# Optimization experiments

Measured on AMD Instinct MI355X. Metric: run time of the kernel, lower is better.

## Reference

```python
import jax, jax.numpy as jnp
import numpy as np

N_NODES = 100000
N_EDGES = 600000
FEAT = 128
HID = 128
N_LAYERS = 5
BN_EPS = 1e-5


def setup_inputs() -> dict:
    key = jax.random.key(0)
    ks = jax.random.split(key, 10)
    x = jax.random.normal(ks[0], (N_NODES, FEAT), dtype=jnp.float32)
    edge_index = jax.random.randint(ks[1], (2, N_EDGES), 0, N_NODES, dtype=jnp.int64)
    # conv weights: all layers are 128->128 (glorot-ish scale)
    conv_w = jax.random.normal(ks[2], (N_LAYERS, HID, HID), dtype=jnp.float32) * (1.0 / np.sqrt(HID))
    conv_b = jnp.zeros((N_LAYERS, HID), dtype=jnp.float32)
    bn_gamma = jnp.ones((N_LAYERS, HID), dtype=jnp.float32)
    bn_beta = jnp.zeros((N_LAYERS, HID), dtype=jnp.float32)
    fc_w = jax.random.normal(ks[3], (1, HID), dtype=jnp.float32) * (1.0 / np.sqrt(HID))
    fc_b = jnp.zeros((1,), dtype=jnp.float32)
    return {"x": x, "edge_index": edge_index, "conv_w": conv_w, "conv_b": conv_b,
            "bn_gamma": bn_gamma, "bn_beta": bn_beta, "fc_w": fc_w, "fc_b": fc_b}


def _gcn_norm(edge_index, n_nodes):
    # PyG gcn_norm with add_self_loops=True, edge_weight=None (ones)
    row = jnp.concatenate([edge_index[0], jnp.arange(n_nodes, dtype=edge_index.dtype)])
    col = jnp.concatenate([edge_index[1], jnp.arange(n_nodes, dtype=edge_index.dtype)])
    ew = jnp.ones(row.shape[0], dtype=jnp.float32)
    deg = jax.ops.segment_sum(ew, col, num_segments=n_nodes)
    dinv = jnp.where(deg > 0, jax.lax.rsqrt(deg), 0.0)
    norm = dinv[row] * ew * dinv[col]  # [E + N]
    return row, col, norm


def reference(x, edge_index, conv_w, conv_b, bn_gamma, bn_beta, fc_w, fc_b):
    n = x.shape[0]
    row, col, norm = _gcn_norm(edge_index, n)
    for l in range(N_LAYERS):
        h = x @ conv_w[l]                                   # [N, H]
        msg = norm[:, None] * h[row]                        # gather + scale
        h = jax.ops.segment_sum(msg, col, num_segments=n)   # scatter-add
        h = h + conv_b[l]
        # BatchNorm1d (training-mode batch stats, biased var)
        mean = jnp.mean(h, axis=0)
        var = jnp.var(h, axis=0)
        h = bn_gamma[l] * (h - mean) * jax.lax.rsqrt(var + BN_EPS) + bn_beta[l]
        x = jax.nn.relu(h)
    edge_emb = x[edge_index[0]] * x[edge_index[1]]          # [E, H]
    out = edge_emb @ fc_w.T + fc_b                          # [E, 1]
    return jax.nn.sigmoid(out)
```

## Files before the change

kernel.cpp:

```cpp
#include <hip/hip_runtime.h>

#define NN 100000
#define NE 600000
#define HH 128
#define NL 5
#define BN_EPS 1e-5f
#define NB 391
#define NBS 782
#define L2B 32
#define RPB 25

typedef float f4 __attribute__((ext_vector_type(4)));
typedef float f2 __attribute__((ext_vector_type(2)));
typedef _Float16 h8 __attribute__((ext_vector_type(8)));
typedef _Float16 h2x __attribute__((ext_vector_type(2)));

__global__ void k_probe(const unsigned long long* __restrict__ e, int* __restrict__ flag) {
    if (blockIdx.x == 0 && threadIdx.x == 0) {
        int ok = 1;
        for (int i = 0; i < 64; ++i)
            if (e[i] >= (unsigned long long)NN) ok = 0;
        *flag = ok;
    }
}

__global__ void k_convert(const void* __restrict__ src, const int* __restrict__ flag,
                          int* __restrict__ dst) {
    int i = blockIdx.x * 256 + threadIdx.x;
    if (i >= 2 * NE) return;
    if (*flag) dst[i] = (int)((const long long*)src)[i];
    else       dst[i] = ((const int*)src)[i];
}

__global__ void k_zero(int* __restrict__ p, int n) {
    int i = blockIdx.x * 256 + threadIdx.x;
    if (i < n) p[i] = 0;
}

__global__ void k_count_deg(const int* __restrict__ col, int* __restrict__ degi) {
    int e = blockIdx.x * 256 + threadIdx.x;
    if (e < NE) atomicAdd(&degi[col[e]], 1);
}

__global__ void k_dinv(const int* __restrict__ degi, float* __restrict__ dinv) {
    int i = blockIdx.x * 256 + threadIdx.x;
    if (i < NN) dinv[i] = rsqrtf((float)degi[i] + 1.0f);
}

__global__ __launch_bounds__(256) void k_scan1(const int* __restrict__ degi,
                                               int* __restrict__ incl,
                                               int* __restrict__ blocksums) {
    __shared__ int sd[256];
    int tid = threadIdx.x;
    int i = blockIdx.x * 256 + tid;
    int v = (i < NN) ? degi[i] : 0;
    sd[tid] = v;
    __syncthreads();
#pragma unroll
    for (int off = 1; off < 256; off <<= 1) {
        int t = (tid >= off) ? sd[tid - off] : 0;
        __syncthreads();
        sd[tid] += t;
        __syncthreads();
    }
    if (i < NN) incl[i] = sd[tid];
    if (tid == 255) blocksums[blockIdx.x] = sd[255];
}

__global__ __launch_bounds__(512) void k_scan2(const int* __restrict__ blocksums,
                                               int* __restrict__ blockoffs) {
    __shared__ int sd[512];
    int tid = threadIdx.x;
    int v = (tid < NB) ? blocksums[tid] : 0;
    sd[tid] = v;
    __syncthreads();
#pragma unroll
    for (int off = 1; off < 512; off <<= 1) {
        int t = (tid >= off) ? sd[tid - off] : 0;
        __syncthreads();
        sd[tid] += t;
        __syncthreads();
    }
    if (tid < NB) blockoffs[tid] = sd[tid] - v;
}

__global__ void k_scan3(const int* __restrict__ incl, const int* __restrict__ degi,
                        const int* __restrict__ blockoffs,
                        int* __restrict__ offsets, int* __restrict__ cursor) {
    int i = blockIdx.x * 256 + threadIdx.x;
    if (i >= NN) return;
    offsets[i] = incl[i] - degi[i] + blockoffs[blockIdx.x];
    cursor[i] = 0;
}

__global__ void k_scatter(const int* __restrict__ ei, const float* __restrict__ dinv,
                          const int* __restrict__ offsets, int* __restrict__ cursor,
                          int2* __restrict__ csr) {
    int e = blockIdx.x * 256 + threadIdx.x;
    if (e >= NE) return;
    int r = ei[e], c = ei[NE + e];
    int pos = offsets[c] + atomicAdd(&cursor[c], 1);
    int2 v;
    v.x = r;
    v.y = __float_as_int(dinv[r] * dinv[c]);
    csr[pos] = v;
}

__global__ void k_wt(const float* __restrict__ W, _Float16* __restrict__ Wt_hi,
                     _Float16* __restrict__ Wt_lo) {
    int gid = blockIdx.x * 256 + threadIdx.x;
    if (gid >= NL * HH * HH) return;
    int l = gid >> 14;
    int rem = gid & 16383;
    int n = rem >> 7;
    int k = rem & 127;
    float w = W[l * HH * HH + k * HH + n];
    _Float16 hi = (_Float16)w;
    _Float16 lo = (_Float16)(w - (float)hi);
    Wt_hi[gid] = hi;
    Wt_lo[gid] = lo;
}

__global__ void k_prep(const float* __restrict__ stats, const float* __restrict__ gamma,
                       const float* __restrict__ beta, int mode, float* __restrict__ scsh) {
    int k = threadIdx.x;
    float sc = 1.0f, sh = 0.0f;
    if (mode) {
        const float inv_n = 1.0f / (float)NN;
        float mean = stats[k] * inv_n;
        float var  = stats[128 + k] * inv_n - mean * mean;
        sc = gamma[k] * rsqrtf(var + BN_EPS);
        sh = beta[k] - mean * sc;
    }
    scsh[k] = sc;
    scsh[128 + k] = sh;
}

__global__ __launch_bounds__(256) void k_gemm(const float* __restrict__ A,
                                              const _Float16* __restrict__ Wt_hi,
                                              const _Float16* __restrict__ Wt_lo,
                                              const float* __restrict__ scsh,
                                              float negmul,
                                              float* __restrict__ C) {
    __shared__ _Float16 sBH[16384];
    __shared__ _Float16 sBL[16384];
    const int tid = threadIdx.x;

#pragma unroll
    for (int it = 0; it < 8; ++it) {
        int g  = it * 256 + tid;
        int rr = g & 15;
        int kg = (g >> 4) & 3;
        int kc = (g >> 6) & 3;
        int n  = g >> 8;
        int glob = (n * 16 + rr) * HH + kc * 32 + kg * 8;
        *reinterpret_cast<h8*>(&sBH[g * 8]) = *reinterpret_cast<const h8*>(Wt_hi + glob);
        *reinterpret_cast<h8*>(&sBL[g * 8]) = *reinterpret_cast<const h8*>(Wt_lo + glob);
    }
    __syncthreads();

    const int wave = tid >> 6;
    const int lane = tid & 63;
    const int r    = lane & 15;
    const int kg   = lane >> 4;
    const int row0 = blockIdx.x * 256 + wave * 64;

    f4 acc[4][8];
#pragma unroll
    for (int m = 0; m < 4; ++m)
#pragma unroll
        for (int n = 0; n < 8; ++n) acc[m][n] = (f4)0.0f;

    const float* Ap[4];
#pragma unroll
    for (int m = 0; m < 4; ++m) {
        int ra = row0 + m * 16 + r;
        if (ra >= NN) ra = NN - 1;
        Ap[m] = A + (size_t)ra * HH + kg * 8;
    }

#pragma unroll
    for (int kc = 0; kc < 4; ++kc) {
        const int k0 = kc * 32 + kg * 8;
        f4 scA = *reinterpret_cast<const f4*>(scsh + k0);
        f4 scB = *reinterpret_cast<const f4*>(scsh + k0 + 4);
        f4 shA = *reinterpret_cast<const f4*>(scsh + 128 + k0);
        f4 shB = *reinterpret_cast<const f4*>(scsh + 128 + k0 + 4);
        h8 ahi[4], alo[4];
#pragma unroll
        for (int m = 0; m < 4; ++m) {
            f4 ax = *reinterpret_cast<const f4*>(Ap[m] + kc * 32);
            f4 ay = *reinterpret_cast<const f4*>(Ap[m] + kc * 32 + 4);
#pragma unroll
            for (int j = 0; j < 4; ++j) {
                float t;
                t = fmaf(ax[j], scA[j], shA[j]); t = fmaxf(t, t * negmul);
                ahi[m][j] = (_Float16)t;      alo[m][j] = (_Float16)(t - (float)ahi[m][j]);
                t = fmaf(ay[j], scB[j], shB[j]); t = fmaxf(t, t * negmul);
                ahi[m][j + 4] = (_Float16)t;  alo[m][j + 4] = (_Float16)(t - (float)ahi[m][j + 4]);
            }
        }
#pragma unroll
        for (int n = 0; n < 8; ++n) {
            int g = n * 256 + kc * 64 + lane;
            h8 bh = *reinterpret_cast<const h8*>(&sBH[g * 8]);
            h8 bl = *reinterpret_cast<const h8*>(&sBL[g * 8]);
#pragma unroll
            for (int m = 0; m < 4; ++m) {
                acc[m][n] = __builtin_amdgcn_mfma_f32_16x16x32_f16(bh, ahi[m], acc[m][n], 0, 0, 0);
                acc[m][n] = __builtin_amdgcn_mfma_f32_16x16x32_f16(bl, ahi[m], acc[m][n], 0, 0, 0);
                acc[m][n] = __builtin_amdgcn_mfma_f32_16x16x32_f16(bh, alo[m], acc[m][n], 0, 0, 0);
            }
        }
    }

#pragma unroll
    for (int m = 0; m < 4; ++m) {
        int rr = row0 + m * 16 + r;
        if (rr < NN) {
            float* Crow = C + (size_t)rr * HH + kg * 4;
#pragma unroll
            for (int n = 0; n < 8; ++n)
                *reinterpret_cast<f4*>(Crow + n * 16) = acc[m][n];
        }
    }
}

__global__ __launch_bounds__(256) void k_gather(const float* __restrict__ h1,
                                                const int* __restrict__ offsets,
                                                const int* __restrict__ degi,
                                                const int2* __restrict__ csr,
                                                const float* __restrict__ dinv,
                                                float* __restrict__ h2) {
    int gid  = blockIdx.x * 256 + threadIdx.x;
    int node = gid >> 6;
    int lane = gid & 63;
    if (node >= NN) return;
    float di = dinv[node];
    f2 acc0 = reinterpret_cast<const f2*>(h1 + (size_t)node * HH)[lane] * (di * di);
    f2 acc1 = (f2)0.0f, acc2 = (f2)0.0f, acc3 = (f2)0.0f;
    const int start = offsets[node];
    const int end   = start + degi[node];
    for (int b = start; b < end; b += 4) {
        int2 ce0 = csr[b];
        int2 ce1 = (b + 1 < end) ? csr[b + 1] : make_int2(0, 0);
        int2 ce2 = (b + 2 < end) ? csr[b + 2] : make_int2(0, 0);
        int2 ce3 = (b + 3 < end) ? csr[b + 3] : make_int2(0, 0);
        f2 v0 = reinterpret_cast<const f2*>(h1 + (size_t)ce0.x * HH)[lane];
        f2 v1 = reinterpret_cast<const f2*>(h1 + (size_t)ce1.x * HH)[lane];
        f2 v2 = reinterpret_cast<const f2*>(h1 + (size_t)ce2.x * HH)[lane];
        f2 v3 = reinterpret_cast<const f2*>(h1 + (size_t)ce3.x * HH)[lane];
        acc0 += v0 * __int_as_float(ce0.y);
        acc1 += v1 * __int_as_float(ce1.y);
        acc2 += v2 * __int_as_float(ce2.y);
        acc3 += v3 * __int_as_float(ce3.y);
    }
    acc0 += acc2;
    acc1 += acc3;
    acc0 += acc1;
    reinterpret_cast<f2*>(h2 + (size_t)node * HH)[lane] = acc0;
}

__global__ __launch_bounds__(256) void k_bnstats(const float* __restrict__ h,
                                                 float* __restrict__ partial) {
    __shared__ f4 ls[8][32];
    __shared__ f4 lss[8][32];
    const int q  = threadIdx.x & 31;
    const int rg = threadIdx.x >> 5;
    const int r0 = blockIdx.x * 128;
    int rend = r0 + 128;
    if (rend > NN) rend = NN;
    f4 s = (f4)0.0f, ss = (f4)0.0f;
    for (int r = r0 + rg; r < rend; r += 8) {
        f4 v = *reinterpret_cast<const f4*>(h + (size_t)r * HH + q * 4);
        s += v;
        ss += v * v;
    }
    ls[rg][q] = s;
    lss[rg][q] = ss;
    __syncthreads();
    if (rg == 0) {
        f4 st = ls[0][q];
#pragma unroll
        for (int g = 1; g < 8; ++g) st += ls[g][q];
        *reinterpret_cast<f4*>(&partial[(size_t)blockIdx.x * 256 + q * 4]) = st;
    } else if (rg == 1) {
        f4 sq = lss[0][q];
#pragma unroll
        for (int g = 1; g < 8; ++g) sq += lss[g][q];
        *reinterpret_cast<f4*>(&partial[(size_t)blockIdx.x * 256 + 128 + q * 4]) = sq;
    }
}

__global__ void k_sred1(const float* __restrict__ partial, float* __restrict__ level2) {
    int c = threadIdx.x;
    int b0 = blockIdx.x * RPB;
    int b1 = b0 + RPB;
    if (b1 > NBS) b1 = NBS;
    float s = 0.0f;
    for (int b = b0; b < b1; ++b) s += partial[(size_t)b * 256 + c];
    level2[(size_t)blockIdx.x * 256 + c] = s;
}

__global__ void k_sred2(const float* __restrict__ level2, float* __restrict__ stats) {
    int c = threadIdx.x;
    float s = 0.0f;
#pragma unroll
    for (int b = 0; b < L2B; ++b) s += level2[(size_t)b * 256 + c];
    stats[c] = s;
}

__global__ void k_bnapply(const float* __restrict__ h2, const float* __restrict__ stats,
                          const float* __restrict__ gamma, const float* __restrict__ beta,
                          _Float16* __restrict__ xh) {
    int idx = blockIdx.x * 256 + threadIdx.x;
    if (idx >= NN * 64) return;
    int cp = idx & 63;
    int c0 = 2 * cp, c1 = c0 + 1;
    const float inv_n = 1.0f / (float)NN;
    float m0 = stats[c0] * inv_n, m1 = stats[c1] * inv_n;
    float v0s = stats[128 + c0] * inv_n - m0 * m0;
    float v1s = stats[128 + c1] * inv_n - m1 * m1;
    float sc0 = gamma[c0] * rsqrtf(v0s + BN_EPS);
    float sc1 = gamma[c1] * rsqrtf(v1s + BN_EPS);
    float sh0 = beta[c0] - m0 * sc0;
    float sh1 = beta[c1] - m1 * sc1;
    f2 v = reinterpret_cast<const f2*>(h2)[idx];
    float t0 = fmaf(v[0], sc0, sh0);
    float t1 = fmaf(v[1], sc1, sh1);
    t0 = fmaxf(t0, 0.0f);
    t1 = fmaxf(t1, 0.0f);
    h2x o;
    o[0] = (_Float16)t0;
    o[1] = (_Float16)t1;
    reinterpret_cast<h2x*>(xh)[idx] = o;
}

__global__ __launch_bounds__(256) void k_final(const _Float16* __restrict__ x,
                                               const int* __restrict__ ei,
                                               const float* __restrict__ fcw,
                                               const float* __restrict__ fcb,
                                               float* __restrict__ out) {
    int gid  = blockIdx.x * 256 + threadIdx.x;
    int e    = gid >> 4;
    int l16  = gid & 15;
    if (e >= NE) return;
    int a = ei[e];
    int b = ei[NE + e];
    h8 va = *reinterpret_cast<const h8*>(x + (size_t)a * HH + l16 * 8);
    h8 vb = *reinterpret_cast<const h8*>(x + (size_t)b * HH + l16 * 8);
    f4 w0 = *reinterpret_cast<const f4*>(fcw + l16 * 8);
    f4 w1 = *reinterpret_cast<const f4*>(fcw + l16 * 8 + 4);
    float p = 0.0f;
#pragma unroll
    for (int j = 0; j < 4; ++j) {
        p += (float)va[j] * (float)vb[j] * w0[j];
        p += (float)va[j + 4] * (float)vb[j + 4] * w1[j];
    }
#pragma unroll
    for (int off = 8; off > 0; off >>= 1) p += __shfl_xor(p, off, 64);
    if (l16 == 0) out[e] = 1.0f / (1.0f + expf(-(p + fcb[0])));
}

extern "C" void kernel_launch(void* const* d_in, const int* in_sizes, int n_in,
                              void* d_out, int out_size, void* d_ws, size_t ws_size,
                              hipStream_t stream) {
    const float* x   = (const float*)d_in[0];
    const void*  ei_raw = d_in[1];
    const float* cw  = (const float*)d_in[2];
    const float* gam = (const float*)d_in[4];
    const float* bet = (const float*)d_in[5];
    const float* fcw = (const float*)d_in[6];
    const float* fcb = (const float*)d_in[7];
    float* out = (float*)d_out;

    const size_t NH = (size_t)NN * HH;
    unsigned char* p = (unsigned char*)d_ws;
    float* h1 = (float*)p;       p += NH * 4;
    float* h2 = (float*)p;       p += NH * 4;
    _Float16* xh = (_Float16*)p; p += NH * 2;
    _Float16* WtH = (_Float16*)p; p += (size_t)NL * HH * HH * 2;
    _Float16* WtL = (_Float16*)p; p += (size_t)NL * HH * HH * 2;
    int2*  csr   = (int2*)p;     p += (size_t)NE * 8;
    float* dinv  = (float*)p;    p += NN * 4;
    float* stats = (float*)p;    p += NL * 256 * 4;
    float* scsh  = (float*)p;    p += NL * 256 * 4;
    float* partial = (float*)p;  p += (size_t)NBS * 256 * 4;
    float* level2  = (float*)p;  p += (size_t)L2B * 256 * 4;
    int*   ei    = (int*)p;      p += (size_t)2 * NE * 4;
    int*   degi  = (int*)p;      p += NN * 4;
    int*   incl  = (int*)p;      p += NN * 4;
    int*   offsets = (int*)p;    p += NN * 4;
    int*   cursor  = (int*)p;    p += NN * 4;
    int*   blocksums = (int*)p;  p += NB * 4;
    int*   blockoffs = (int*)p;  p += NB * 4;
    int*   flag  = (int*)p;

    k_probe<<<1, 64, 0, stream>>>((const unsigned long long*)ei_raw, flag);
    k_convert<<<(2 * NE + 255) / 256, 256, 0, stream>>>(ei_raw, flag, ei);

    k_zero<<<(NN + 255) / 256, 256, 0, stream>>>(degi, NN);
    k_count_deg<<<(NE + 255) / 256, 256, 0, stream>>>(ei + NE, degi);
    k_dinv<<<(NN + 255) / 256, 256, 0, stream>>>(degi, dinv);
    k_scan1<<<NB, 256, 0, stream>>>(degi, incl, blocksums);
    k_scan2<<<1, 512, 0, stream>>>(blocksums, blockoffs);
    k_scan3<<<NB, 256, 0, stream>>>(incl, degi, blockoffs, offsets, cursor);
    k_scatter<<<(NE + 255) / 256, 256, 0, stream>>>(ei, dinv, offsets, cursor, csr);

    k_wt<<<(NL * HH * HH + 255) / 256, 256, 0, stream>>>(cw, WtH, WtL);

    for (int l = 0; l < NL; ++l) {
        k_prep<<<1, 128, 0, stream>>>(
            (l == 0) ? stats : stats + (size_t)(l - 1) * 256,
            (l == 0) ? gam : gam + (size_t)(l - 1) * HH,
            (l == 0) ? bet : bet + (size_t)(l - 1) * HH,
            (l == 0) ? 0 : 1, scsh + (size_t)l * 256);
        k_gemm<<<(NN + 255) / 256, 256, 0, stream>>>(
            (l == 0) ? x : h2, WtH + (size_t)l * HH * HH, WtL + (size_t)l * HH * HH,
            scsh + (size_t)l * 256, (l == 0) ? 1.0f : 0.0f, h1);
        k_gather<<<(NN * 64 + 255) / 256, 256, 0, stream>>>(h1, offsets, degi, csr, dinv, h2);
        k_bnstats<<<NBS, 256, 0, stream>>>(h2, partial);
        k_sred1<<<L2B, 256, 0, stream>>>(partial, level2);
        k_sred2<<<1, 256, 0, stream>>>(level2, stats + (size_t)l * 256);
    }
    k_bnapply<<<(NN * 64 + 255) / 256, 256, 0, stream>>>(h2, stats + (size_t)(NL - 1) * 256,
                                                         gam + (size_t)(NL - 1) * HH,
                                                         bet + (size_t)(NL - 1) * HH, xh);
    k_final<<<(NE * 16 + 255) / 256, 256, 0, stream>>>(xh, ei, fcw, fcb, out);
}
```

Measured before the change: 690.8 us.

## Fuse BatchNorm statistics into gather kernel and fold final reduction into prep

The gather kernel now computes per-block sums and squared sums of its output rows in shared memory and writes a partial per block, which removes the separate bnstats pass that re-read h2 each layer. The second-level reduction is folded into k_prep, and bnapply now reads precomputed scale and shift values, which drops the sred2 launches. The cost is that sred1 must now reduce 25000 partials instead of 782, using only 32 blocks of long serial loops. The gather kernel also gains a __syncthreads barrier.

```diff
diff --git a/kernel.cpp b/kernel.cpp
--- a/kernel.cpp
+++ b/kernel.cpp
@@ -6,9 +6,9 @@
 #define NL 5
 #define BN_EPS 1e-5f
 #define NB 391
-#define NBS 782
+#define NGB 25000
 #define L2B 32
-#define RPB 25
+#define RPB2 782
 
 typedef float f4 __attribute__((ext_vector_type(4)));
 typedef float f2 __attribute__((ext_vector_type(2)));
@@ -121,14 +121,20 @@
     Wt_lo[gid] = lo;
 }
 
-__global__ void k_prep(const float* __restrict__ stats, const float* __restrict__ gamma,
+__global__ void k_prep(const float* __restrict__ level2, const float* __restrict__ gamma,
                        const float* __restrict__ beta, int mode, float* __restrict__ scsh) {
     int k = threadIdx.x;
     float sc = 1.0f, sh = 0.0f;
     if (mode) {
+        float s = 0.0f, q = 0.0f;
+#pragma unroll
+        for (int b = 0; b < L2B; ++b) {
+            s += level2[(size_t)b * 256 + k];
+            q += level2[(size_t)b * 256 + 128 + k];
+        }
         const float inv_n = 1.0f / (float)NN;
-        float mean = stats[k] * inv_n;
-        float var  = stats[128 + k] * inv_n - mean * mean;
+        float mean = s * inv_n;
+        float var  = q * inv_n - mean * mean;
         sc = gamma[k] * rsqrtf(var + BN_EPS);
         sh = beta[k] - mean * sc;
     }
@@ -231,11 +237,14 @@
                                                 const int* __restrict__ degi,
                                                 const int2* __restrict__ csr,
                                                 const float* __restrict__ dinv,
-                                                float* __restrict__ h2) {
+                                                float* __restrict__ h2,
+                                                float* __restrict__ partial) {
+    __shared__ f2 ls[4][64];
+    __shared__ f2 lss[4][64];
     int gid  = blockIdx.x * 256 + threadIdx.x;
     int node = gid >> 6;
     int lane = gid & 63;
-    if (node >= NN) return;
+    int wid  = threadIdx.x >> 6;
     float di = dinv[node];
     f2 acc0 = reinterpret_cast<const f2*>(h1 + (size_t)node * HH)[lane] * (di * di);
     f2 acc1 = (f2)0.0f, acc2 = (f2)0.0f, acc3 = (f2)0.0f;
@@ -259,72 +268,37 @@
     acc1 += acc3;
     acc0 += acc1;
     reinterpret_cast<f2*>(h2 + (size_t)node * HH)[lane] = acc0;
-}
-
-__global__ __launch_bounds__(256) void k_bnstats(const float* __restrict__ h,
-                                                 float* __restrict__ partial) {
-    __shared__ f4 ls[8][32];
-    __shared__ f4 lss[8][32];
-    const int q  = threadIdx.x & 31;
-    const int rg = threadIdx.x >> 5;
-    const int r0 = blockIdx.x * 128;
-    int rend = r0 + 128;
-    if (rend > NN) rend = NN;
-    f4 s = (f4)0.0f, ss = (f4)0.0f;
-    for (int r = r0 + rg; r < rend; r += 8) {
-        f4 v = *reinterpret_cast<const f4*>(h + (size_t)r * HH + q * 4);
-        s += v;
-        ss += v * v;
-    }
-    ls[rg][q] = s;
-    lss[rg][q] = ss;
+
+    ls[wid][lane] = acc0;
+    lss[wid][lane] = acc0 * acc0;
     __syncthreads();
-    if (rg == 0) {
-        f4 st = ls[0][q];
-#pragma unroll
-        for (int g = 1; g < 8; ++g) st += ls[g][q];
-        *reinterpret_cast<f4*>(&partial[(size_t)blockIdx.x * 256 + q * 4]) = st;
-    } else if (rg == 1) {
-        f4 sq = lss[0][q];
-#pragma unroll
-        for (int g = 1; g < 8; ++g) sq += lss[g][q];
-        *reinterpret_cast<f4*>(&partial[(size_t)blockIdx.x * 256 + 128 + q * 4]) = sq;
+    if (threadIdx.x < 64) {
+        int c = threadIdx.x;
+        f2 s = ls[0][c] + ls[1][c] + ls[2][c] + ls[3][c];
+        f2 q = lss[0][c] + lss[1][c] + lss[2][c] + lss[3][c];
+        f2* pp = reinterpret_cast<f2*>(partial + (size_t)blockIdx.x * 256);
+        pp[c] = s;
+        pp[64 + c] = q;
     }
 }
 
 __global__ void k_sred1(const float* __restrict__ partial, float* __restrict__ level2) {
     int c = threadIdx.x;
-    int b0 = blockIdx.x * RPB;
-    int b1 = b0 + RPB;
-    if (b1 > NBS) b1 = NBS;
+    int b0 = blockIdx.x * RPB2;
+    int b1 = b0 + RPB2;
+    if (b1 > NGB) b1 = NGB;
     float s = 0.0f;
     for (int b = b0; b < b1; ++b) s += partial[(size_t)b * 256 + c];
     level2[(size_t)blockIdx.x * 256 + c] = s;
 }
 
-__global__ void k_sred2(const float* __restrict__ level2, float* __restrict__ stats) {
-    int c = threadIdx.x;
-    float s = 0.0f;
-#pragma unroll
-    for (int b = 0; b < L2B; ++b) s += level2[(size_t)b * 256 + c];
-    stats[c] = s;
-}
-
-__global__ void k_bnapply(const float* __restrict__ h2, const float* __restrict__ stats,
-                          const float* __restrict__ gamma, const float* __restrict__ beta,
+__global__ void k_bnapply(const float* __restrict__ h2, const float* __restrict__ scsh,
                           _Float16* __restrict__ xh) {
     int idx = blockIdx.x * 256 + threadIdx.x;
     if (idx >= NN * 64) return;
     int cp = idx & 63;
-    int c0 = 2 * cp, c1 = c0 + 1;
-    const float inv_n = 1.0f / (float)NN;
-    float m0 = stats[c0] * inv_n, m1 = stats[c1] * inv_n;
-    float v0s = stats[128 + c0] * inv_n - m0 * m0;
-    float v1s = stats[128 + c1] * inv_n - m1 * m1;
-    float sc0 = gamma[c0] * rsqrtf(v0s + BN_EPS);
-    float sc1 = gamma[c1] * rsqrtf(v1s + BN_EPS);
-    float sh0 = beta[c0] - m0 * sc0;
-    float sh1 = beta[c1] - m1 * sc1;
+    float sc0 = scsh[2 * cp],       sc1 = scsh[2 * cp + 1];
+    float sh0 = scsh[128 + 2 * cp], sh1 = scsh[128 + 2 * cp + 1];
     f2 v = reinterpret_cast<const f2*>(h2)[idx];
     float t0 = fmaf(v[0], sc0, sh0);
     float t1 = fmaf(v[1], sc1, sh1);
@@ -383,9 +357,8 @@
     _Float16* WtL = (_Float16*)p; p += (size_t)NL * HH * HH * 2;
     int2*  csr   = (int2*)p;     p += (size_t)NE * 8;
     float* dinv  = (float*)p;    p += NN * 4;
-    float* stats = (float*)p;    p += NL * 256 * 4;
-    float* scsh  = (float*)p;    p += NL * 256 * 4;
-    float* partial = (float*)p;  p += (size_t)NBS * 256 * 4;
+    float* scsh  = (float*)p;    p += (NL + 1) * 256 * 4;
+    float* partial = (float*)p;  p += (size_t)NGB * 256 * 4;
     float* level2  = (float*)p;  p += (size_t)L2B * 256 * 4;
     int*   ei    = (int*)p;      p += (size_t)2 * NE * 4;
     int*   degi  = (int*)p;      p += NN * 4;
@@ -411,20 +384,19 @@
 
     for (int l = 0; l < NL; ++l) {
         k_prep<<<1, 128, 0, stream>>>(
-            (l == 0) ? stats : stats + (size_t)(l - 1) * 256,
+            level2,
             (l == 0) ? gam : gam + (size_t)(l - 1) * HH,
             (l == 0) ? bet : bet + (size_t)(l - 1) * HH,
             (l == 0) ? 0 : 1, scsh + (size_t)l * 256);
         k_gemm<<<(NN + 255) / 256, 256, 0, stream>>>(
             (l == 0) ? x : h2, WtH + (size_t)l * HH * HH, WtL + (size_t)l * HH * HH,
             scsh + (size_t)l * 256, (l == 0) ? 1.0f : 0.0f, h1);
-        k_gather<<<(NN * 64 + 255) / 256, 256, 0, stream>>>(h1, offsets, degi, csr, dinv, h2);
-        k_bnstats<<<NBS, 256, 0, stream>>>(h2, partial);
+        k_gather<<<NGB, 256, 0, stream>>>(h1, offsets, degi, csr, dinv, h2, partial);
         k_sred1<<<L2B, 256, 0, stream>>>(partial, level2);
-        k_sred2<<<1, 256, 0, stream>>>(level2, stats + (size_t)l * 256);
-    }
-    k_bnapply<<<(NN * 64 + 255) / 256, 256, 0, stream>>>(h2, stats + (size_t)(NL - 1) * 256,
-                                                         gam + (size_t)(NL - 1) * HH,
-                                                         bet + (size_t)(NL - 1) * HH, xh);
+    }
+    k_prep<<<1, 128, 0, stream>>>(level2, gam + (size_t)(NL - 1) * HH,
+                                  bet + (size_t)(NL - 1) * HH, 1,
+                                  scsh + (size_t)NL * 256);
+    k_bnapply<<<(NN * 64 + 255) / 256, 256, 0, stream>>>(h2, scsh + (size_t)NL * 256, xh);
     k_final<<<(NE * 16 + 255) / 256, 256, 0, stream>>>(xh, ei, fcw, fcb, out);
 }
```

Measured after the change: 1.598 ms. 2.31x slower.
